# Optimization experiments

Measured on AMD Instinct MI355X. Metric: run time of the kernel, lower is better.

The kernel has to match this reference:

```python
import jax, jax.numpy as jnp
import numpy as np

EPS = 1e-5

def layer_norm(x, w, b):
    mu = x.mean(-1, keepdims=True)
    var = x.var(-1, keepdims=True)
    return (x - mu) / jnp.sqrt(var + EPS) * w + b

def s5_forward(u, Lambda_re, Lambda_im, B_re, B_im, C_re, C_im, D, log_step):
    # u: [B, L, H]; diagonal S5 SSM with P complex states, ZOH discretization.
    Lam = (Lambda_re + 1j * Lambda_im).astype(jnp.complex64)          # [P]
    dt = jnp.exp(log_step).astype(jnp.complex64)                       # [P]
    Lam_bar = jnp.exp(Lam * dt)                                        # [P]
    Bc = (B_re + 1j * B_im).astype(jnp.complex64)                      # [P, H]
    B_bar = ((Lam_bar - 1.0) / Lam)[:, None] * Bc                      # [P, H]
    Bu = jnp.einsum('blh,ph->blp', u.astype(jnp.complex64), B_bar)     # [B, L, P]
    A = jnp.broadcast_to(Lam_bar, Bu.shape)                            # [B, L, P]

    def binop(e1, e2):
        a1, b1 = e1
        a2, b2 = e2
        return (a2 * a1, a2 * b1 + b2)

    _, xs = jax.lax.associative_scan(binop, (A, Bu), axis=1)           # [B, L, P]
    Cc = (C_re + 1j * C_im).astype(jnp.complex64)                      # [H, P]
    y = 2.0 * jnp.einsum('blp,hp->blh', xs, Cc).real + D * u           # [B, L, H]
    return y

def setup_inputs() -> dict:
    key = jax.random.key(0)
    ks = jax.random.split(key, 12)
    B, L, H, P = 4, 4096, 512, 512
    x = jax.random.normal(ks[0], (B, L, H), jnp.float32)
    # SSM params (HiPPO-like flavor: negative real part, spread imaginary part)
    Lambda_re = -(0.5 * jax.random.uniform(ks[1], (P,), jnp.float32) + 0.1)
    Lambda_im = jnp.pi * jnp.arange(P, dtype=jnp.float32)
    B_re = jax.random.normal(ks[2], (P, H), jnp.float32) / np.sqrt(2.0 * H)
    B_im = jax.random.normal(ks[3], (P, H), jnp.float32) / np.sqrt(2.0 * H)
    C_re = jax.random.normal(ks[4], (H, P), jnp.float32) / np.sqrt(P)
    C_im = jax.random.normal(ks[5], (H, P), jnp.float32) / np.sqrt(P)
    D = jax.random.normal(ks[6], (H,), jnp.float32)
    log_step = jax.random.uniform(ks[7], (P,), jnp.float32,
                                  minval=np.log(1e-3), maxval=np.log(1e-1))
    ln1_w = jnp.ones((H,), jnp.float32); ln1_b = jnp.zeros((H,), jnp.float32)
    ln2_w = jnp.ones((H,), jnp.float32); ln2_b = jnp.zeros((H,), jnp.float32)
    W_enc = jax.random.normal(ks[8], (2 * H, H), jnp.float32) / np.sqrt(H)
    W_dec = jax.random.normal(ks[9], (H, H), jnp.float32) / np.sqrt(H)
    return {"x": x, "ln1_w": ln1_w, "ln1_b": ln1_b,
            "Lambda_re": Lambda_re, "Lambda_im": Lambda_im,
            "B_re": B_re, "B_im": B_im, "C_re": C_re, "C_im": C_im,
            "D": D, "log_step": log_step,
            "ln2_w": ln2_w, "ln2_b": ln2_b, "W_enc": W_enc, "W_dec": W_dec}

def reference(x, ln1_w, ln1_b, Lambda_re, Lambda_im, B_re, B_im, C_re, C_im,
              D, log_step, ln2_w, ln2_b, W_enc, W_dec):
    fx = layer_norm(x, ln1_w, ln1_b)
    res = fx
    u = s5_forward(fx, Lambda_re, Lambda_im, B_re, B_im, C_re, C_im, D, log_step)
    h = jax.nn.gelu(u, approximate=False) + res  # eval mode: dropout = identity
    fx2 = layer_norm(h, ln2_w, ln2_b)
    e = fx2 @ W_enc.T                              # [B, L, 2H]
    a, g = jnp.split(e, 2, axis=-1)
    ff = a * jax.nn.gelu(g, approximate=False)     # GEGLU
    out = ff @ W_dec.T + fx2
    return out
```

## Files before the change

kernel.cpp:

```cpp
#include <hip/hip_runtime.h>
#include <math.h>

#define Bz 4
#define Lz 4096
#define Hz 512
#define Pz 512
#define Nz (Bz*Lz)
#define CL 64
#define NC (Lz/CL)
#define CS (Bz*NC*Pz)
#define EPSf 1e-5f

typedef unsigned short u16;
typedef unsigned int   u32;
typedef __attribute__((ext_vector_type(8))) short bf16x8;
typedef __attribute__((ext_vector_type(4))) float f32x4;

__device__ __forceinline__ float gelu_exact(float x){
    return 0.5f * x * (1.0f + erff(x * 0.70710678118654752f));
}
__device__ __forceinline__ u16 f2b(float f){
    union { float f; u32 u; } v; v.f = f;
    u32 u = v.u;
    u32 r = (u + 0x7FFFu + ((u >> 16) & 1u)) >> 16;
    return (u16)r;
}
__device__ __forceinline__ float b2f(u16 h){
    union { u32 u; float f; } v; v.u = ((u32)h) << 16; return v.f;
}
__device__ __forceinline__ float cvt_in(float x){ return x; }
__device__ __forceinline__ float cvt_in(u16 x){ return b2f(x); }

__device__ __forceinline__ void gload_lds16(const u16* g, u16* l){
    __builtin_amdgcn_global_load_lds(
        (const __attribute__((address_space(1))) void*)g,
        (__attribute__((address_space(3))) void*)l, 16, 0, 0);
}

__global__ void setup_kernel(const float* __restrict__ Lre, const float* __restrict__ Lim,
                             const float* __restrict__ log_step,
                             float* __restrict__ prm){
    int p = blockIdx.x*blockDim.x + threadIdx.x;
    if (p >= Pz) return;
    float lr = Lre[p], li = Lim[p];
    float dt = expf(log_step[p]);
    float ar = lr*dt, ai = li*dt;
    float e = expf(ar);
    float Abr = e*cosf(ai), Abi = e*sinf(ai);
    prm[p]        = Abr;
    prm[Pz + p]   = Abi;
    float nr = Abr - 1.0f, ni = Abi;
    float d2 = lr*lr + li*li;
    prm[2*Pz + p] = (nr*lr + ni*li)/d2;
    prm[3*Pz + p] = (ni*lr - nr*li)/d2;
    float arC = ar*(float)CL, aiC = ai*(float)CL;
    float eC = expf(arC);
    prm[4*Pz + p] = eC*cosf(aiC);
    prm[5*Pz + p] = eC*sinf(aiC);
}

__global__ __launch_bounds__(256) void cvt_all(const float* __restrict__ B_re,
                                               const float* __restrict__ B_im,
                                               const float* __restrict__ C_re,
                                               const float* __restrict__ C_im,
                                               const float* __restrict__ W_enc,
                                               const float* __restrict__ W_dec,
                                               u16* __restrict__ Bcat,
                                               u16* __restrict__ Ccat,
                                               u16* __restrict__ Wenc,
                                               u16* __restrict__ Wdec){
    const int Q = 512*512;
    int i = blockIdx.x*256 + threadIdx.x;
    if (i < Q){ Bcat[i] = f2b(B_re[i]); return; }
    i -= Q;
    if (i < Q){ Bcat[Q + i] = f2b(B_im[i]); return; }
    i -= Q;
    if (i < Q){
        int h = i >> 9, p = i & 511;
        Ccat[(size_t)h*1024 + p]       = f2b(C_re[i]);
        Ccat[(size_t)h*1024 + 512 + p] = f2b(-C_im[i]);
        return;
    }
    i -= Q;
    if (i < 2*Q){ Wenc[i] = f2b(W_enc[i]); return; }
    i -= 2*Q;
    Wdec[i] = f2b(W_dec[i]);
}

template<typename T>
__global__ __launch_bounds__(256) void ln_kernel(const T* __restrict__ in,
                                                 const float* __restrict__ w,
                                                 const float* __restrict__ b,
                                                 u16* __restrict__ ob){
    int row = blockIdx.x;
    int tid = threadIdx.x;
    const T* r = in + (size_t)row*Hz;
    float v0 = cvt_in(r[tid]), v1 = cvt_in(r[tid+256]);
    float s = v0+v1, q = v0*v0+v1*v1;
    #pragma unroll
    for (int o=32;o;o>>=1){ s += __shfl_down(s,o); q += __shfl_down(q,o); }
    __shared__ float ss[4], sq[4];
    __shared__ float mu_s, rs_s;
    int wid = tid>>6, lane = tid&63;
    if (lane==0){ ss[wid]=s; sq[wid]=q; }
    __syncthreads();
    if (tid==0){
        float S=ss[0]+ss[1]+ss[2]+ss[3];
        float Q=sq[0]+sq[1]+sq[2]+sq[3];
        float mu = S/(float)Hz;
        float var = Q/(float)Hz - mu*mu;
        mu_s = mu; rs_s = rsqrtf(var + EPSf);
    }
    __syncthreads();
    float mu = mu_s, rs = rs_s;
    u16* o = ob + (size_t)row*Hz;
    o[tid]     = f2b((v0-mu)*rs*w[tid]    +b[tid]);
    o[tid+256] = f2b((v1-mu)*rs*w[tid+256]+b[tid+256]);
}

#define EB16 0
#define EY   1
#define ERES 2

__device__ __forceinline__ void stage128(const u16* __restrict__ src, int ld,
                                         int grow0, int kt, u16* lds){
    int lane = threadIdx.x & 63;
    int w    = threadIdx.x >> 6;
    #pragma unroll
    for (int q = 0; q < 4; ++q){
        int c = w + q*4;
        int r = c*8 + (lane >> 3);
        int colE = 8*((lane & 7) ^ ((lane >> 3) & 7));
        const u16* g = src + (size_t)(grow0 + r)*ld + kt + colE;
        gload_lds16(g, lds + c*512);
    }
}

template<int K, int EPI>
__global__ __launch_bounds__(256, 2)
void gemm2p(const u16* __restrict__ A, const u16* __restrict__ Bw, int M,
            u16* __restrict__ outB,
            const u16* __restrict__ fxB,
            const float* __restrict__ Dv,
            const u16* __restrict__ resB,
            float* __restrict__ outF)
{
    constexpr int NT = K/64;
    __shared__ u16 AL[2][128*64];
    __shared__ u16 BL[2][128*64];

    int nx = gridDim.x, ny = gridDim.y;
    int nwg = nx*ny;
    int lid = blockIdx.x + blockIdx.y*nx;
    int cpx = nwg >> 3;
    int gdx = (lid & 7)*cpx + (lid >> 3);
    int n0 = (gdx / ny) * 128;
    int m0 = (gdx % ny) * 128;

    int l = threadIdx.x & 63;
    int w = threadIdx.x >> 6;
    int lrow  = l & 15;
    int lcol0 = ((l >> 4)*8) ^ ((l & 7) << 3);
    int lcol1 = lcol0 ^ 32;
    int colw  = w*32;

    f32x4 acc[8][2];
    #pragma unroll
    for (int i=0;i<8;++i){ acc[i][0]=(f32x4)(0.f); acc[i][1]=(f32x4)(0.f); }

    stage128(A,  K, n0, 0, &AL[0][0]);
    stage128(Bw, K, m0, 0, &BL[0][0]);
    __syncthreads();

    for (int T=0; T<NT; ++T){
        int buf = T & 1, nb = buf ^ 1;
        if (T+1 < NT){
            int ktn = (T+1)*64;
            stage128(A,  K, n0, ktn, &AL[nb][0]);
            stage128(Bw, K, m0, ktn, &BL[nb][0]);
        }
        const u16* Ab = &AL[buf][0];
        const u16* Bb = &BL[buf][0];
        bf16x8 bfr[2][2];
        #pragma unroll
        for (int fn=0; fn<2; ++fn){
            bfr[0][fn] = *(const bf16x8*)&Bb[(colw + fn*16 + lrow)*64 + lcol0];
            bfr[1][fn] = *(const bf16x8*)&Bb[(colw + fn*16 + lrow)*64 + lcol1];
        }
        #pragma unroll
        for (int f=0; f<8; ++f){
            bf16x8 a0 = *(const bf16x8*)&Ab[(f*16 + lrow)*64 + lcol0];
            bf16x8 a1 = *(const bf16x8*)&Ab[(f*16 + lrow)*64 + lcol1];
            #pragma unroll
            for (int fn=0; fn<2; ++fn){
                acc[f][fn] = __builtin_amdgcn_mfma_f32_16x16x32_bf16(a0, bfr[0][fn], acc[f][fn], 0,0,0);
                acc[f][fn] = __builtin_amdgcn_mfma_f32_16x16x32_bf16(a1, bfr[1][fn], acc[f][fn], 0,0,0);
            }
        }
        __syncthreads();
    }

    int er = (l >> 4) * 4;
    int ec = l & 15;
    #pragma unroll
    for (int fm=0; fm<8; ++fm)
        #pragma unroll
        for (int fn=0; fn<2; ++fn)
            #pragma unroll
            for (int q=0; q<4; ++q){
                int n = n0 + fm*16 + er + q;
                int m = m0 + colw + fn*16 + ec;
                float v = acc[fm][fn][q];
                if (EPI == EB16){
                    outB[(size_t)n*M + m] = f2b(v);
                } else if (EPI == EY){
                    size_t idx = (size_t)n*Hz + m;
                    float fxv = b2f(fxB[idx]);
                    float y = 2.0f*v + Dv[m]*fxv;
                    outB[idx] = f2b(gelu_exact(y) + fxv);
                } else {
                    size_t idx = (size_t)n*Hz + m;
                    outF[idx] = v + b2f(resB[idx]);
                }
            }
}

__global__ __launch_bounds__(256) void scan_phase1(const u16* __restrict__ g,
                                                   const float* __restrict__ prm,
                                                   float* __restrict__ ERe,
                                                   float* __restrict__ EIm){
    int t = blockIdx.x;
    int pb = t & 1; t >>= 1;
    int c  = t % NC; t /= NC;
    int b  = t;
    int p  = pb*256 + threadIdx.x;
    size_t base = ((size_t)(b*Lz + c*CL))*1024 + p;
    float Ar = prm[p], Ai = prm[Pz+p];
    float fre = prm[2*Pz+p], fim = prm[3*Pz+p];
    float xr = 0.f, xi = 0.f;
    for (int ll = 0; ll < CL; ++ll) {
        float gr = b2f(g[base]), gi = b2f(g[base+512]);
        float br = fre*gr - fim*gi;
        float bi = fre*gi + fim*gr;
        float nr = Ar*xr - Ai*xi + br;
        float ni = Ar*xi + Ai*xr + bi;
        xr = nr; xi = ni;
        base += 1024;
    }
    size_t ci = ((size_t)(b*NC + c))*Pz + p;
    ERe[ci] = xr; EIm[ci] = xi;
}

__global__ __launch_bounds__(256) void scan_combine(const float* __restrict__ ERe,
                                                    const float* __restrict__ EIm,
                                                    const float* __restrict__ prm,
                                                    float* __restrict__ SinRe,
                                                    float* __restrict__ SinIm){
    int gt = blockIdx.x*256 + threadIdx.x;
    int b = gt / Pz, p = gt % Pz;
    float Ar = prm[4*Pz+p], Ai = prm[5*Pz+p];
    float Sr = 0.f, Si = 0.f;
    for (int c = 0; c < NC; ++c) {
        size_t idx = ((size_t)(b*NC + c))*Pz + p;
        SinRe[idx] = Sr; SinIm[idx] = Si;
        float er = ERe[idx], ei = EIm[idx];
        float nr = Ar*Sr - Ai*Si + er;
        float ni = Ar*Si + Ai*Sr + ei;
        Sr = nr; Si = ni;
    }
}

__global__ __launch_bounds__(256) void scan_phase2(u16* __restrict__ g,
                                                   const float* __restrict__ prm,
                                                   const float* __restrict__ SinRe,
                                                   const float* __restrict__ SinIm){
    int t = blockIdx.x;
    int pb = t & 1; t >>= 1;
    int c  = t % NC; t /= NC;
    int b  = t;
    int p  = pb*256 + threadIdx.x;
    size_t base = ((size_t)(b*Lz + c*CL))*1024 + p;
    size_t ci = ((size_t)(b*NC + c))*Pz + p;
    float Ar = prm[p], Ai = prm[Pz+p];
    float fre = prm[2*Pz+p], fim = prm[3*Pz+p];
    float xr = SinRe[ci], xi = SinIm[ci];
    for (int ll = 0; ll < CL; ++ll) {
        float gr = b2f(g[base]), gi = b2f(g[base+512]);
        float br = fre*gr - fim*gi;
        float bi = fre*gi + fim*gr;
        float nr = Ar*xr - Ai*xi + br;
        float ni = Ar*xi + Ai*xr + bi;
        xr = nr; xi = ni;
        g[base] = f2b(xr); g[base+512] = f2b(xi);
        base += 1024;
    }
}

__global__ __launch_bounds__(256) void geglu_kernel(const u16* __restrict__ e,
                                                    u16* __restrict__ ff){
    size_t i = (size_t)blockIdx.x*256 + threadIdx.x;
    int n = (int)(i >> 9), m = (int)(i & 511);
    float a = b2f(e[(size_t)n*1024 + m]);
    float gg = b2f(e[(size_t)n*1024 + 512 + m]);
    ff[i] = f2b(a * gelu_exact(gg));
}

extern "C" void kernel_launch(void* const* d_in, const int* in_sizes, int n_in,
                              void* d_out, int out_size, void* d_ws, size_t ws_size,
                              hipStream_t stream) {
    const float* x        = (const float*)d_in[0];
    const float* ln1_w    = (const float*)d_in[1];
    const float* ln1_b    = (const float*)d_in[2];
    const float* Lre      = (const float*)d_in[3];
    const float* Lim      = (const float*)d_in[4];
    const float* B_re     = (const float*)d_in[5];
    const float* B_im     = (const float*)d_in[6];
    const float* C_re     = (const float*)d_in[7];
    const float* C_im     = (const float*)d_in[8];
    const float* Dv       = (const float*)d_in[9];
    const float* log_step = (const float*)d_in[10];
    const float* ln2_w    = (const float*)d_in[11];
    const float* ln2_b    = (const float*)d_in[12];
    const float* W_enc    = (const float*)d_in[13];
    const float* W_dec    = (const float*)d_in[14];
    float* out = (float*)d_out;

    const size_t NH = (size_t)Nz*Hz;
    char* W = (char*)d_ws;
    u16*   fxb  = (u16*)  (W);
    u16*   g    = (u16*)  (W + NH*2);
    u16*   hb   = (u16*)  (W + NH*6);
    u16*   fx2b = (u16*)  (W + NH*8);
    float* ERe  = (float*)(W + NH*10);
    float* EIm  = ERe + CS;
    float* SinRe= EIm + CS;
    float* SinIm= SinRe + CS;
    float* prm  = SinIm + CS;
    u16*   Bcat = (u16*)(prm + 6*Pz);
    u16*   Ccat = Bcat + 1024*512;
    u16*   Wenc = Ccat + 512*1024;
    u16*   Wdec = Wenc + 1024*512;

    setup_kernel<<<dim3(2), dim3(256), 0, stream>>>(Lre, Lim, log_step, prm);

    cvt_all<<<dim3(6*1024), dim3(256), 0, stream>>>(B_re, B_im, C_re, C_im, W_enc, W_dec,
                                                    Bcat, Ccat, Wenc, Wdec);

    ln_kernel<float><<<dim3(Nz), dim3(256), 0, stream>>>(x, ln1_w, ln1_b, fxb);

    gemm2p<512,EB16><<<dim3(Nz/128, 1024/128), dim3(256), 0, stream>>>(
        fxb, Bcat, 1024, g, nullptr, nullptr, nullptr, nullptr);

    scan_phase1<<<dim3(Bz*NC*2), dim3(256), 0, stream>>>(g, prm, ERe, EIm);
    scan_combine<<<dim3((Bz*Pz)/256), dim3(256), 0, stream>>>(ERe, EIm, prm, SinRe, SinIm);
    scan_phase2<<<dim3(Bz*NC*2), dim3(256), 0, stream>>>(g, prm, SinRe, SinIm);

    gemm2p<1024,EY><<<dim3(Nz/128, 512/128), dim3(256), 0, stream>>>(
        g, Ccat, 512, hb, fxb, Dv, nullptr, nullptr);

    ln_kernel<u16><<<dim3(Nz), dim3(256), 0, stream>>>(hb, ln2_w, ln2_b, fx2b);

    gemm2p<512,EB16><<<dim3(Nz/128, 1024/128), dim3(256), 0, stream>>>(
        fx2b, Wenc, 1024, g, nullptr, nullptr, nullptr, nullptr);

    geglu_kernel<<<dim3((unsigned)(NH/256)), dim3(256), 0, stream>>>(g, fxb);

    gemm2p<512,ERES><<<dim3(Nz/128, 512/128), dim3(256), 0, stream>>>(
        fxb, Wdec, 512, nullptr, nullptr, nullptr, fx2b, out);
}
```

Measured before the change: 189.3 us.

## Fuse GEGLU into encoder GEMM epilogue and shrink GEMM K-tile to 32

Interleaves the rows of W_enc so the value and gate columns for each output sit next to each other. The encoder GEMM epilogue can then pair them with a lane shuffle and write the GEGLU result directly. This removes the separate geglu kernel and the round trip of the 2H-wide intermediate through memory. Separately, every GEMM now uses a 32-wide K tile with half the LDS, a re-derived swizzle and launch bounds raised to 4 blocks per CU. The smaller tile means twice as many loop iterations and barriers per GEMM.

```diff
diff --git a/kernel.cpp b/kernel.cpp
--- a/kernel.cpp
+++ b/kernel.cpp
@@ -82,8 +82,18 @@
         return;
     }
     i -= Q;
-    if (i < 2*Q){ Wenc[i] = f2b(W_enc[i]); return; }
-    i -= 2*Q;
+    if (i < Q){
+        int t = i >> 9, col = i & 511;
+        Wenc[(size_t)(2*t)*512 + col] = f2b(W_enc[i]);
+        return;
+    }
+    i -= Q;
+    if (i < Q){
+        int t = i >> 9, col = i & 511;
+        Wenc[(size_t)(2*t+1)*512 + col] = f2b(W_enc[Q + i]);
+        return;
+    }
+    i -= Q;
     Wdec[i] = f2b(W_dec[i]);
 }
 
@@ -121,33 +131,34 @@
 #define EB16 0
 #define EY   1
 #define ERES 2
-
-__device__ __forceinline__ void stage128(const u16* __restrict__ src, int ld,
-                                         int grow0, int kt, u16* lds){
+#define EGLU 3
+
+__device__ __forceinline__ void stage32(const u16* __restrict__ src, int ld,
+                                        int grow0, int kt, u16* lds){
     int lane = threadIdx.x & 63;
     int w    = threadIdx.x >> 6;
     #pragma unroll
-    for (int q = 0; q < 4; ++q){
+    for (int q = 0; q < 2; ++q){
         int c = w + q*4;
-        int r = c*8 + (lane >> 3);
-        int colE = 8*((lane & 7) ^ ((lane >> 3) & 7));
+        int r = c*16 + (lane >> 2);
+        int colE = 8*((lane & 3) ^ ((lane >> 3) & 3));
         const u16* g = src + (size_t)(grow0 + r)*ld + kt + colE;
         gload_lds16(g, lds + c*512);
     }
 }
 
 template<int K, int EPI>
-__global__ __launch_bounds__(256, 2)
-void gemm2p(const u16* __restrict__ A, const u16* __restrict__ Bw, int M,
-            u16* __restrict__ outB,
-            const u16* __restrict__ fxB,
-            const float* __restrict__ Dv,
-            const u16* __restrict__ resB,
-            float* __restrict__ outF)
+__global__ __launch_bounds__(256, 4)
+void gemmk(const u16* __restrict__ A, const u16* __restrict__ Bw, int M,
+           u16* __restrict__ outB,
+           const u16* __restrict__ fxB,
+           const float* __restrict__ Dv,
+           const u16* __restrict__ resB,
+           float* __restrict__ outF)
 {
-    constexpr int NT = K/64;
-    __shared__ u16 AL[2][128*64];
-    __shared__ u16 BL[2][128*64];
+    constexpr int NT = K/32;
+    __shared__ u16 AL[2][128*32];
+    __shared__ u16 BL[2][128*32];
 
     int nx = gridDim.x, ny = gridDim.y;
     int nwg = nx*ny;
@@ -159,43 +170,37 @@
 
     int l = threadIdx.x & 63;
     int w = threadIdx.x >> 6;
-    int lrow  = l & 15;
-    int lcol0 = ((l >> 4)*8) ^ ((l & 7) << 3);
-    int lcol1 = lcol0 ^ 32;
-    int colw  = w*32;
+    int lrow = l & 15;
+    int lcol = 8*((l >> 4) ^ ((l >> 1) & 3));
+    int colw = w*32;
 
     f32x4 acc[8][2];
     #pragma unroll
     for (int i=0;i<8;++i){ acc[i][0]=(f32x4)(0.f); acc[i][1]=(f32x4)(0.f); }
 
-    stage128(A,  K, n0, 0, &AL[0][0]);
-    stage128(Bw, K, m0, 0, &BL[0][0]);
+    stage32(A,  K, n0, 0, &AL[0][0]);
+    stage32(Bw, K, m0, 0, &BL[0][0]);
     __syncthreads();
 
     for (int T=0; T<NT; ++T){
         int buf = T & 1, nb = buf ^ 1;
         if (T+1 < NT){
-            int ktn = (T+1)*64;
-            stage128(A,  K, n0, ktn, &AL[nb][0]);
-            stage128(Bw, K, m0, ktn, &BL[nb][0]);
+            int ktn = (T+1)*32;
+            stage32(A,  K, n0, ktn, &AL[nb][0]);
+            stage32(Bw, K, m0, ktn, &BL[nb][0]);
         }
         const u16* Ab = &AL[buf][0];
         const u16* Bb = &BL[buf][0];
-        bf16x8 bfr[2][2];
+        bf16x8 bfr[2];
         #pragma unroll
-        for (int fn=0; fn<2; ++fn){
-            bfr[0][fn] = *(const bf16x8*)&Bb[(colw + fn*16 + lrow)*64 + lcol0];
-            bfr[1][fn] = *(const bf16x8*)&Bb[(colw + fn*16 + lrow)*64 + lcol1];
-        }
+        for (int fn=0; fn<2; ++fn)
+            bfr[fn] = *(const bf16x8*)&Bb[(colw + fn*16 + lrow)*32 + lcol];
         #pragma unroll
         for (int f=0; f<8; ++f){
-            bf16x8 a0 = *(const bf16x8*)&Ab[(f*16 + lrow)*64 + lcol0];
-            bf16x8 a1 = *(const bf16x8*)&Ab[(f*16 + lrow)*64 + lcol1];
+            bf16x8 af = *(const bf16x8*)&Ab[(f*16 + lrow)*32 + lcol];
             #pragma unroll
-            for (int fn=0; fn<2; ++fn){
-                acc[f][fn] = __builtin_amdgcn_mfma_f32_16x16x32_bf16(a0, bfr[0][fn], acc[f][fn], 0,0,0);
-                acc[f][fn] = __builtin_amdgcn_mfma_f32_16x16x32_bf16(a1, bfr[1][fn], acc[f][fn], 0,0,0);
-            }
+            for (int fn=0; fn<2; ++fn)
+                acc[f][fn] = __builtin_amdgcn_mfma_f32_16x16x32_bf16(af, bfr[fn], acc[f][fn], 0,0,0);
         }
         __syncthreads();
     }
@@ -218,9 +223,15 @@
                     float fxv = b2f(fxB[idx]);
                     float y = 2.0f*v + Dv[m]*fxv;
                     outB[idx] = f2b(gelu_exact(y) + fxv);
-                } else {
+                } else if (EPI == ERES){
                     size_t idx = (size_t)n*Hz + m;
                     outF[idx] = v + b2f(resB[idx]);
+                } else {
+                    float p = __shfl_xor(v, 1);
+                    if (!(ec & 1)){
+                        float ffv = v * gelu_exact(p);
+                        outB[(size_t)n*Hz + (m >> 1)] = f2b(ffv);
+                    }
                 }
             }
 }
@@ -296,15 +307,6 @@
     }
 }
 
-__global__ __launch_bounds__(256) void geglu_kernel(const u16* __restrict__ e,
-                                                    u16* __restrict__ ff){
-    size_t i = (size_t)blockIdx.x*256 + threadIdx.x;
-    int n = (int)(i >> 9), m = (int)(i & 511);
-    float a = b2f(e[(size_t)n*1024 + m]);
-    float gg = b2f(e[(size_t)n*1024 + 512 + m]);
-    ff[i] = f2b(a * gelu_exact(gg));
-}
-
 extern "C" void kernel_launch(void* const* d_in, const int* in_sizes, int n_in,
                               void* d_out, int out_size, void* d_ws, size_t ws_size,
                               hipStream_t stream) {
@@ -348,23 +350,21 @@
 
     ln_kernel<float><<<dim3(Nz), dim3(256), 0, stream>>>(x, ln1_w, ln1_b, fxb);
 
-    gemm2p<512,EB16><<<dim3(Nz/128, 1024/128), dim3(256), 0, stream>>>(
+    gemmk<512,EB16><<<dim3(Nz/128, 1024/128), dim3(256), 0, stream>>>(
         fxb, Bcat, 1024, g, nullptr, nullptr, nullptr, nullptr);
 
     scan_phase1<<<dim3(Bz*NC*2), dim3(256), 0, stream>>>(g, prm, ERe, EIm);
     scan_combine<<<dim3((Bz*Pz)/256), dim3(256), 0, stream>>>(ERe, EIm, prm, SinRe, SinIm);
     scan_phase2<<<dim3(Bz*NC*2), dim3(256), 0, stream>>>(g, prm, SinRe, SinIm);
 
-    gemm2p<1024,EY><<<dim3(Nz/128, 512/128), dim3(256), 0, stream>>>(
+    gemmk<1024,EY><<<dim3(Nz/128, 512/128), dim3(256), 0, stream>>>(
         g, Ccat, 512, hb, fxb, Dv, nullptr, nullptr);
 
     ln_kernel<u16><<<dim3(Nz), dim3(256), 0, stream>>>(hb, ln2_w, ln2_b, fx2b);
 
-    gemm2p<512,EB16><<<dim3(Nz/128, 1024/128), dim3(256), 0, stream>>>(
-        fx2b, Wenc, 1024, g, nullptr, nullptr, nullptr, nullptr);
-
-    geglu_kernel<<<dim3((unsigned)(NH/256)), dim3(256), 0, stream>>>(g, fxb);
-
-    gemm2p<512,ERES><<<dim3(Nz/128, 512/128), dim3(256), 0, stream>>>(
+    gemmk<512,EGLU><<<dim3(Nz/128, 1024/128), dim3(256), 0, stream>>>(
+        fx2b, Wenc, 1024, fxb, nullptr, nullptr, nullptr, nullptr);
+
+    gemmk<512,ERES><<<dim3(Nz/128, 512/128), dim3(256), 0, stream>>>(
         fxb, Wdec, 512, nullptr, nullptr, nullptr, fx2b, out);
 }
```

Measured after the change: 210.0 us. 10.9% more time.
